# Performance work log

Hardware: AMD Instinct MI355X
Metric: run time of the kernel (lower is better)

## Reference

```python
import jax, jax.numpy as jnp
import numpy as np

LMAX = 10
F_IN = 64
F_OUT = 64
N_GRID = 512
B = 512


def setup_inputs() -> dict:
    key = jax.random.key(0)
    k1, k2, k3 = jax.random.split(key, 3)
    x = jax.random.normal(k1, (B, F_IN, (LMAX + 1) ** 2), dtype=jnp.float32)
    w = jax.random.normal(k2, (F_IN, F_OUT, N_GRID), dtype=jnp.float32)
    Y = jax.random.normal(k3, (N_GRID, (LMAX + 1) ** 2), dtype=jnp.float32)
    return {"x": x, "w": w, "Y": Y}


def reference(x, w, Y):
    # Project spatial filter into harmonic (fourier) domain.
    # psi: (f_in, f_out, (lmax+1)^2), one scalar weight per (l, u) output mult slot
    n_grid = Y.shape[0]
    psi = jnp.einsum('ni,xyn->xyi', Y, w) / (n_grid ** 0.5)

    lmax = int(round(Y.shape[1] ** 0.5)) - 1
    f_in = w.shape[0]
    f_out = w.shape[1]
    alpha = 1.0 / (f_in ** 0.5)  # e3nn Linear path normalization (mul_in=1)

    outs = []
    for l in range(lmax + 1):  # structural loop over irrep degrees (11 blocks)
        d = 2 * l + 1
        xs = x[:, :, l * l:(l + 1) * (l + 1)]     # (B, f_in, d)  single input copy of irrep l
        ws = psi[:, :, l * l:(l + 1) * (l + 1)]    # (f_in, f_out, d) -> d = output multiplicity u
        # out block: (B, f_out, mult=d, m=d)
        o = jnp.einsum('egu,bem->bgum', ws, xs) * alpha
        outs.append(o.reshape(x.shape[0], f_out, d * d))
    return jnp.concatenate(outs, axis=-1)  # (B, f_out, sum_l (2l+1)^2)
```

## Files before the change

### kernel.cpp

```cpp
#include <hip/hip_runtime.h>
#include <hip/hip_bf16.h>


#define OUTROW 1771
#define OUTB   113344

typedef __attribute__((ext_vector_type(8))) short bf16x8;
typedef __attribute__((ext_vector_type(4))) float floatx4;

__device__ __constant__ int c_off[11] = {0,1,10,35,84,165,286,455,680,969,1330};
__device__ __constant__ signed char c_ltab[121] = {
  0,
  1,1,1,
  2,2,2,2,2,
  3,3,3,3,3,3,3,
  4,4,4,4,4,4,4,4,4,
  5,5,5,5,5,5,5,5,5,5,5,
  6,6,6,6,6,6,6,6,6,6,6,6,6,
  7,7,7,7,7,7,7,7,7,7,7,7,7,7,7,
  8,8,8,8,8,8,8,8,8,8,8,8,8,8,8,8,8,
  9,9,9,9,9,9,9,9,9,9,9,9,9,9,9,9,9,9,9,
  10,10,10,10,10,10,10,10,10,10,10,10,10,10,10,10,10,10,10,10,10
};

__global__ __launch_bounds__(256) void prep_kernel(
    const float* __restrict__ x, const float* __restrict__ w,
    const float* __restrict__ Y,
    __hip_bfloat16* __restrict__ psi_t, __hip_bfloat16* __restrict__ x_t)
{
  __shared__ float smem[8256];
  const int t = threadIdx.x;

  if (blockIdx.x < 64) {
    const int g    = blockIdx.x;
    const int wv   = t >> 6, lane = t & 63;
    const int ln15 = lane & 15, quad = lane >> 4;

    floatx4 acc[2][4] = {};

    for (int n0 = 0; n0 < 512; n0 += 64) {
      __syncthreads();
      {
        const float4* src = (const float4*)(Y + n0*121);
        float4* dst = (float4*)smem;
        for (int idx = t; idx < 1936; idx += 256) dst[idx] = src[idx];
      }
      __syncthreads();

      #pragma unroll
      for (int ks = 0; ks < 2; ++ks) {
        const int kb = ks*32 + quad*8;

        bf16x8 ahi[2], alo[2];
        #pragma unroll
        for (int ti = 0; ti < 2; ++ti) {
          const int irow = (wv << 5) + (ti << 4) + ln15;
          #pragma unroll
          for (int j = 0; j < 8; ++j) {
            float v = smem[(kb + j)*121 + irow];
            __hip_bfloat16 h = __float2bfloat16(v);
            float hf = __bfloat162float(h);
            __hip_bfloat16 lo = __float2bfloat16(v - hf);
            ahi[ti][j] = *(short*)&h;
            alo[ti][j] = *(short*)&lo;
          }
        }

        bf16x8 bhi[4], blo[4];
        #pragma unroll
        for (int te = 0; te < 4; ++te) {
          const int e = (te << 4) + ln15;
          const float* wp = w + ((e << 6) + g)*512 + n0 + kb;
          float4 wa = *(const float4*)wp;
          float4 wb = *(const float4*)(wp + 4);
          float v[8] = {wa.x, wa.y, wa.z, wa.w, wb.x, wb.y, wb.z, wb.w};
          #pragma unroll
          for (int j = 0; j < 8; ++j) {
            __hip_bfloat16 h = __float2bfloat16(v[j]);
            float hf = __bfloat162float(h);
            __hip_bfloat16 lo = __float2bfloat16(v[j] - hf);
            bhi[te][j] = *(short*)&h;
            blo[te][j] = *(short*)&lo;
          }
        }

        #pragma unroll
        for (int ti = 0; ti < 2; ++ti) {
          #pragma unroll
          for (int te = 0; te < 4; ++te) {
            acc[ti][te] = __builtin_amdgcn_mfma_f32_16x16x32_bf16(ahi[ti], bhi[te], acc[ti][te], 0, 0, 0);
            acc[ti][te] = __builtin_amdgcn_mfma_f32_16x16x32_bf16(ahi[ti], blo[te], acc[ti][te], 0, 0, 0);
            acc[ti][te] = __builtin_amdgcn_mfma_f32_16x16x32_bf16(alo[ti], bhi[te], acc[ti][te], 0, 0, 0);
          }
        }
      }
    }

    const float scale = 0.00552427172801990267f;
    #pragma unroll
    for (int ti = 0; ti < 2; ++ti) {
      #pragma unroll
      for (int rr = 0; rr < 4; ++rr) {
        const int i = (wv << 5) + (ti << 4) + (quad << 2) + rr;
        if (i < 121) {
          int l = c_ltab[i];
          int d = 2*l + 1;
          int row = 64*l*l + g*d + (i - l*l);
          #pragma unroll
          for (int te = 0; te < 4; ++te) {
            __hip_bfloat16 hv = __float2bfloat16(acc[ti][te][rr] * scale);
            psi_t[row*64 + (te << 4) + ln15] = hv;
          }
        }
      }
    }
  } else {
    const int b = blockIdx.x - 64;
    {
      const float4* src = (const float4*)(x + b*7744);
      float4* dst = (float4*)smem;
      for (int idx = t; idx < 1936; idx += 256) dst[idx] = src[idx];
    }
    __syncthreads();
    const int wv = t >> 6, lane = t & 63;
    for (int ii = wv; ii < 121; ii += 4) {
      int l = c_ltab[ii];
      int d = 2*l + 1;
      int row = 512*l*l + b*d + (ii - l*l);
      x_t[row*64 + lane] = __float2bfloat16(smem[lane*121 + ii]);
    }
  }
}

__global__ __launch_bounds__(256) void conv_kernel(
    const __hip_bfloat16* __restrict__ psi_t,
    const __hip_bfloat16* __restrict__ x_t,
    float* __restrict__ out)
{
  const int bid = blockIdx.x;
  int l = 0;
  #pragma unroll
  for (int ll = 1; ll <= 10; ++ll)
    if (bid >= 2*c_off[ll]) l = ll;
  const int d = 2*l + 1;
  const int r = bid - 2*c_off[l];
  const int qtiles = 2*d;
  const int ptile = r / qtiles;
  const int qtile = r - ptile*qtiles;
  const int p0 = ptile*64, q0 = qtile*256;

  const int t = threadIdx.x;
  const int wv = t >> 6, lane = t & 63;
  const int ln15 = lane & 15, quad = lane >> 4;
  const int pw = p0 + wv*16;

  const ushort* psiRow = (const ushort*)psi_t + (64*l*l + pw + ln15)*64 + quad*8;
  const bf16x8 af0 = *(const bf16x8*)(psiRow);
  const bf16x8 af1 = *(const bf16x8*)(psiRow + 32);

  int rowoff[4];
  #pragma unroll
  for (int rr = 0; rr < 4; ++rr) {
    int p  = pw + quad*4 + rr;
    int gg = p / d;
    int uu = p - gg*d;
    rowoff[rr] = gg*OUTROW + uu*d;
  }
  const int offl = c_off[l];
  const ushort* xbase = (const ushort*)x_t + 512*l*l*64 + quad*8;

  const int stepd = 16 / d;
  const int stepm = 16 - stepd*d;
  int qlane = q0 + ln15;
  int bb = qlane / d;
  int mm = qlane - bb*d;

  #pragma unroll 4
  for (int qq = 0; qq < 16; ++qq) {
    const ushort* xr = xbase + (q0 + qq*16 + ln15)*64;
    bf16x8 bf0 = *(const bf16x8*)(xr);
    bf16x8 bf1 = *(const bf16x8*)(xr + 32);
    floatx4 acc = {0.f, 0.f, 0.f, 0.f};
    acc = __builtin_amdgcn_mfma_f32_16x16x32_bf16(af0, bf0, acc, 0, 0, 0);
    acc = __builtin_amdgcn_mfma_f32_16x16x32_bf16(af1, bf1, acc, 0, 0, 0);
    const int base = bb*OUTB + offl + mm;
    #pragma unroll
    for (int rr = 0; rr < 4; ++rr)
      out[base + rowoff[rr]] = acc[rr];
    bb += stepd; mm += stepm;
    if (mm >= d) { mm -= d; ++bb; }
  }
}

extern "C" void kernel_launch(void* const* d_in, const int* in_sizes, int n_in,
                              void* d_out, int out_size, void* d_ws, size_t ws_size,
                              hipStream_t stream) {
  const float* x = (const float*)d_in[0];
  const float* w = (const float*)d_in[1];
  const float* Y = (const float*)d_in[2];
  float* out = (float*)d_out;

  __hip_bfloat16* psi_t = (__hip_bfloat16*)d_ws;
  __hip_bfloat16* x_t   = (__hip_bfloat16*)((char*)d_ws + (1 << 20));

  prep_kernel<<<576, 256, 0, stream>>>(x, w, Y, psi_t, x_t);
  conv_kernel<<<3542, 256, 0, stream>>>(psi_t, x_t, out);
}
```

Before: 355.0 us.

## Stage conv tiles in LDS for contiguous output stores, specialize per degree

The conv kernel now tiles over whole (g, b) groups, so each block covers complete d×d output blocks. MFMA results are written to a shared-memory tile first and then stored to global memory as contiguous runs per (b, g), replacing the strided scattered stores. The per-degree body is templated on L so divisions become constants, and block IDs are remapped to group neighbouring work on the same XCD. In exchange the kernel uses about 66 KB of LDS per block, needs an extra barrier, and launches more blocks with partially padded tiles.

```diff
diff --git a/kernel.cpp b/kernel.cpp
--- a/kernel.cpp
+++ b/kernel.cpp
@@ -8,7 +8,7 @@
 typedef __attribute__((ext_vector_type(8))) short bf16x8;
 typedef __attribute__((ext_vector_type(4))) float floatx4;
 
-__device__ __constant__ int c_off[11] = {0,1,10,35,84,165,286,455,680,969,1330};
+__device__ __constant__ int c_blk[12] = {0,2,30,96,216,406,705,1137,1633,2403,3283,4229};
 __device__ __constant__ signed char c_ltab[121] = {
   0,
   1,1,1,
@@ -132,63 +132,122 @@
   }
 }
 
+#define LPITCH 258
+
+template <int L>
+__device__ void conv_body(int r, int t,
+                          const ushort* __restrict__ psi,
+                          const ushort* __restrict__ xt,
+                          float* __restrict__ out, float* lt)
+{
+  constexpr int d    = 2*L + 1;
+  constexpr int dd   = d*d;
+  constexpr int GT   = 64  / d;
+  constexpr int BT   = 256 / d;
+  constexpr int NBT  = (512 + BT - 1) / BT;
+  constexpr int OFFL = L*(2*L - 1)*(2*L + 1)/3;
+
+  const int wv = t >> 6, lane = t & 63;
+  const int ln15 = lane & 15, quad = lane >> 4;
+
+  const int gtI = r / NBT;
+  const int btI = r - gtI*NBT;
+  const int g0 = gtI*GT, b0 = btI*BT;
+
+  int pr = g0*d + wv*16 + ln15;
+  if (pr > 64*d - 1) pr = 64*d - 1;
+  const ushort* psiRow = psi + (64*L*L + pr)*64 + quad*8;
+  const bf16x8 af0 = *(const bf16x8*)(psiRow);
+  const bf16x8 af1 = *(const bf16x8*)(psiRow + 32);
+
+  const ushort* xbase = xt + 512*L*L*64 + quad*8;
+
+  #pragma unroll 4
+  for (int qq = 0; qq < 16; ++qq) {
+    int qr = b0*d + qq*16 + ln15;
+    if (qr > 512*d - 1) qr = 512*d - 1;
+    const ushort* xr = xbase + qr*64;
+    bf16x8 bf0 = *(const bf16x8*)(xr);
+    bf16x8 bf1 = *(const bf16x8*)(xr + 32);
+    floatx4 acc = {0.f, 0.f, 0.f, 0.f};
+    acc = __builtin_amdgcn_mfma_f32_16x16x32_bf16(af0, bf0, acc, 0, 0, 0);
+    acc = __builtin_amdgcn_mfma_f32_16x16x32_bf16(af1, bf1, acc, 0, 0, 0);
+    float* dst = lt + (wv*16 + quad*4)*LPITCH + qq*16 + ln15;
+    #pragma unroll
+    for (int rr = 0; rr < 4; ++rr) dst[rr*LPITCH] = acc[rr];
+  }
+  __syncthreads();
+
+  if constexpr (dd >= 64) {
+    for (int pp = wv; pp < GT*BT; pp += 4) {
+      const int g_i = pp / BT;
+      const int b_i = pp - g_i*BT;
+      const int g = g0 + g_i, b = b0 + b_i;
+      if (g >= 64 || b >= 512) continue;
+      const int obase = b*OUTB + g*OUTROW + OFFL;
+      const float* lrow = lt + (g_i*d)*LPITCH + b_i*d;
+      #pragma unroll
+      for (int o0 = 0; o0 < dd; o0 += 64) {
+        int o = o0 + lane;
+        if (o < dd) {
+          int u = o / d;
+          int m = o - u*d;
+          out[obase + o] = lrow[u*LPITCH + m];
+        }
+      }
+    }
+  } else {
+    constexpr int PPI = 64 / dd;
+    const int pq = lane / dd;
+    const int o  = lane - pq*dd;
+    const int u  = o / d;
+    const int m  = o - u*d;
+    for (int base = wv*PPI; base < GT*BT; base += 4*PPI) {
+      int pp = base + pq;
+      if (pq < PPI && pp < GT*BT) {
+        int g_i = pp / BT;
+        int b_i = pp - g_i*BT;
+        int g = g0 + g_i, b = b0 + b_i;
+        if (g < 64 && b < 512)
+          out[b*OUTB + g*OUTROW + OFFL + o] = lt[(g_i*d + u)*LPITCH + b_i*d + m];
+      }
+    }
+  }
+}
+
 __global__ __launch_bounds__(256) void conv_kernel(
     const __hip_bfloat16* __restrict__ psi_t,
     const __hip_bfloat16* __restrict__ x_t,
     float* __restrict__ out)
 {
-  const int bid = blockIdx.x;
+  __shared__ float lt[64*LPITCH];
+
+  const int orig = blockIdx.x;
+  const int xcd = orig & 7, idx = orig >> 3;
+  const int bid = (xcd < 5 ? xcd*529 : 2645 + (xcd - 5)*528) + idx;
+
   int l = 0;
   #pragma unroll
   for (int ll = 1; ll <= 10; ++ll)
-    if (bid >= 2*c_off[ll]) l = ll;
-  const int d = 2*l + 1;
-  const int r = bid - 2*c_off[l];
-  const int qtiles = 2*d;
-  const int ptile = r / qtiles;
-  const int qtile = r - ptile*qtiles;
-  const int p0 = ptile*64, q0 = qtile*256;
-
+    if (bid >= c_blk[ll]) l = ll;
+  const int r = bid - c_blk[l];
+
+  const ushort* psi = (const ushort*)psi_t;
+  const ushort* xt  = (const ushort*)x_t;
   const int t = threadIdx.x;
-  const int wv = t >> 6, lane = t & 63;
-  const int ln15 = lane & 15, quad = lane >> 4;
-  const int pw = p0 + wv*16;
-
-  const ushort* psiRow = (const ushort*)psi_t + (64*l*l + pw + ln15)*64 + quad*8;
-  const bf16x8 af0 = *(const bf16x8*)(psiRow);
-  const bf16x8 af1 = *(const bf16x8*)(psiRow + 32);
-
-  int rowoff[4];
-  #pragma unroll
-  for (int rr = 0; rr < 4; ++rr) {
-    int p  = pw + quad*4 + rr;
-    int gg = p / d;
-    int uu = p - gg*d;
-    rowoff[rr] = gg*OUTROW + uu*d;
-  }
-  const int offl = c_off[l];
-  const ushort* xbase = (const ushort*)x_t + 512*l*l*64 + quad*8;
-
-  const int stepd = 16 / d;
-  const int stepm = 16 - stepd*d;
-  int qlane = q0 + ln15;
-  int bb = qlane / d;
-  int mm = qlane - bb*d;
-
-  #pragma unroll 4
-  for (int qq = 0; qq < 16; ++qq) {
-    const ushort* xr = xbase + (q0 + qq*16 + ln15)*64;
-    bf16x8 bf0 = *(const bf16x8*)(xr);
-    bf16x8 bf1 = *(const bf16x8*)(xr + 32);
-    floatx4 acc = {0.f, 0.f, 0.f, 0.f};
-    acc = __builtin_amdgcn_mfma_f32_16x16x32_bf16(af0, bf0, acc, 0, 0, 0);
-    acc = __builtin_amdgcn_mfma_f32_16x16x32_bf16(af1, bf1, acc, 0, 0, 0);
-    const int base = bb*OUTB + offl + mm;
-    #pragma unroll
-    for (int rr = 0; rr < 4; ++rr)
-      out[base + rowoff[rr]] = acc[rr];
-    bb += stepd; mm += stepm;
-    if (mm >= d) { mm -= d; ++bb; }
+
+  switch (l) {
+    case 0:  conv_body<0 >(r, t, psi, xt, out, lt); break;
+    case 1:  conv_body<1 >(r, t, psi, xt, out, lt); break;
+    case 2:  conv_body<2 >(r, t, psi, xt, out, lt); break;
+    case 3:  conv_body<3 >(r, t, psi, xt, out, lt); break;
+    case 4:  conv_body<4 >(r, t, psi, xt, out, lt); break;
+    case 5:  conv_body<5 >(r, t, psi, xt, out, lt); break;
+    case 6:  conv_body<6 >(r, t, psi, xt, out, lt); break;
+    case 7:  conv_body<7 >(r, t, psi, xt, out, lt); break;
+    case 8:  conv_body<8 >(r, t, psi, xt, out, lt); break;
+    case 9:  conv_body<9 >(r, t, psi, xt, out, lt); break;
+    default: conv_body<10>(r, t, psi, xt, out, lt); break;
   }
 }
 
@@ -204,5 +263,5 @@
   __hip_bfloat16* x_t   = (__hip_bfloat16*)((char*)d_ws + (1 << 20));
 
   prep_kernel<<<576, 256, 0, stream>>>(x, w, Y, psi_t, x_t);
-  conv_kernel<<<3542, 256, 0, stream>>>(psi_t, x_t, out);
-}
+  conv_kernel<<<4229, 256, 0, stream>>>(psi_t, x_t, out);
+}
```

After: 376.1 us. 1.06x slower.
